# Optimization experiments

Measured on AMD Instinct MI355X. Metric: run time of the kernel, lower is better.

## Reference

```python
import jax, jax.numpy as jnp
import numpy as np

N_R = 256          # number of relations
N_HOP_MAX = 3      # max hops
N_E = 200_000      # number of entities
N_T = 1_000_000    # number of KB triples
B = 32             # batch size
D_Q = 768          # BERT question embedding dim
D_IN = D_Q + (N_HOP_MAX - 1) * N_R  # input width of dense_inf / dense_att


def setup_inputs() -> dict:
    key = jax.random.key(0)
    ks = jax.random.split(key, 7)
    x = (jax.random.uniform(ks[0], (B, N_E)) < 0.001).astype(jnp.float32)
    h_q = jax.random.normal(ks[1], (B, D_Q), jnp.float32)
    W_inf = jax.random.normal(ks[2], (N_R, D_IN), jnp.float32) * 0.02
    W_att = jax.random.normal(ks[3], (1, D_IN), jnp.float32) * 0.02
    subj_idx = jax.random.randint(ks[4], (N_T,), 0, N_E, jnp.int32)
    rel_idx = jax.random.randint(ks[5], (N_T,), 0, N_R, jnp.int32)
    obj_idx = jax.random.randint(ks[6], (N_T,), 0, N_E, jnp.int32)
    return {"x": x, "h_q": h_q, "W_inf": W_inf, "W_att": W_att,
            "subj_idx": subj_idx, "rel_idx": rel_idx, "obj_idx": obj_idx,
            "n_hop": N_HOP_MAX}


def _one_step(x, r, subj_idx, rel_idx, obj_idx):
    # Equivalent to ((x @ M_subj.T) * (r @ M_rel.T)) @ M_obj with 0/1
    # indicator matrices: gather - elementwise multiply - scatter-add.
    x_t = jnp.take(x, subj_idx, axis=1)   # (B, N_T)
    r_t = jnp.take(r, rel_idx, axis=1)    # (B, N_T)
    prod = x_t * r_t                       # (B, N_T)
    # scatter-add over triples into object entities: (N_T, B) -> (N_E, B)
    return jax.ops.segment_sum(prod.T, obj_idx, num_segments=x.shape[1]).T


def reference(x, h_q, W_inf, W_att, subj_idx, rel_idx, obj_idx, n_hop):
    rs, cs, xs = [], [], []
    for i in range(n_hop):
        if i:
            # most-recent relation first, then older ones (rs[::-1])
            concat = jnp.concatenate([h_q] + rs[::-1], axis=1)
        else:
            concat = h_q
        pad = jnp.zeros((h_q.shape[0], (N_HOP_MAX - 1 - i) * N_R), h_q.dtype)
        concat = jnp.concatenate([concat, pad], axis=1)  # (B, D_IN)
        r = concat @ W_inf.T   # (B, N_R)
        c = concat @ W_att.T   # (B, 1)
        x = _one_step(x, r, subj_idx, rel_idx, obj_idx)  # (B, N_E)
        rs.append(r)
        cs.append(c)
        xs.append(x)
    a = jax.nn.softmax(jnp.concatenate(cs, axis=1), axis=-1)  # (B, n_hop)
    y = jnp.einsum('bh,bhe->be', a, jnp.stack(xs, axis=1))     # (B, N_E)
    return y
```

## Files before the change

kernel.cpp:

```cpp
#include <hip/hip_runtime.h>

#define N_R   256
#define N_E   200000
#define N_T   1000000
#define D_Q   768
#define D_IN  1280

template <bool BN>
__device__ __forceinline__ void hop_core(
        const float* __restrict__ xIn, const unsigned* __restrict__ maskIn,
        const float* __restrict__ rT,
        const int* __restrict__ subj, const int* __restrict__ rel,
        const int* __restrict__ obj,
        float* __restrict__ xOut, unsigned* __restrict__ maskOut,
        int gb, int nGroups, int t) {
    int stride = nGroups * 256;
    for (int i = gb * 256 + t; i < N_T; i += stride) {
        int s = __builtin_nontemporal_load(&subj[i]);
        unsigned m = maskIn[s];
        if (!m) continue;
        int r = __builtin_nontemporal_load(&rel[i]);
        int o = __builtin_nontemporal_load(&obj[i]);
        const float* rrow = rT + r * 32;
        unsigned mm = m;
        while (mm) {
            int bb = __ffs(mm) - 1;
            mm &= mm - 1;
            float v = BN ? xIn[(size_t)bb * N_E + s] : xIn[(size_t)s * 32 + bb];
            unsafeAtomicAdd(&xOut[(size_t)o * 32 + bb], v * rrow[bb]);
        }
        atomicOr(&maskOut[o], m);
    }
}

__global__ void kA(const float* __restrict__ x, const float* __restrict__ h_q,
                   const float* __restrict__ W_inf,
                   unsigned* __restrict__ mask0, unsigned* __restrict__ mask1,
                   unsigned* __restrict__ mask2,
                   float4* __restrict__ outv, float* __restrict__ rT0) {
    __shared__ float hs[32 * 257];
    __shared__ float red[256];
    int t = threadIdx.x;
    if (blockIdx.x < 782) {
        int tid = blockIdx.x * 256 + t;
        float4 z = {0.f, 0.f, 0.f, 0.f};
        for (int i = tid; i < 1600000; i += 782 * 256) outv[i] = z;
        if (tid < N_E) {
            unsigned m = 0;
#pragma unroll 8
            for (int b = 0; b < 32; ++b)
                m |= (x[(size_t)b * N_E + tid] != 0.f ? 1u : 0u) << b;
            mask0[tid] = m;
            mask1[tid] = 0u;
            mask2[tid] = 0u;
        }
    } else {
        int rel = blockIdx.x - 782;
        int b = t & 31, kp = t >> 5;
        float acc = 0.f;
        for (int c = 0; c < 3; ++c) {
            __syncthreads();
#pragma unroll
            for (int i = 0; i < 32; ++i)
                hs[i * 257 + t] = h_q[i * D_Q + c * 256 + t];
            __syncthreads();
            const float* w = &W_inf[rel * D_IN + c * 256 + kp * 32];
#pragma unroll
            for (int i = 0; i < 32; ++i)
                acc += w[i] * hs[b * 257 + kp * 32 + i];
        }
        red[t] = acc;
        __syncthreads();
        if (t < 32) {
            float s = 0.f;
            for (int q = 0; q < 8; ++q) s += red[q * 32 + t];
            rT0[rel * 32 + t] = s;
        }
    }
}

__global__ void kB(const float* __restrict__ W_inf, const float* __restrict__ rT0,
                   float* __restrict__ rT1,
                   const float* __restrict__ x, const unsigned* __restrict__ mask0,
                   const int* __restrict__ subj, const int* __restrict__ rel,
                   const int* __restrict__ obj,
                   float* __restrict__ bufA, unsigned* __restrict__ mask1) {
    __shared__ float red[256];
    int t = threadIdx.x;
    if (blockIdx.x < 256) {
        int relb = blockIdx.x;
        int b = t & 31, jp = t >> 5;
        const float* w2 = &W_inf[relb * D_IN + D_Q];
        float acc = 0.f;
#pragma unroll 8
        for (int jj = 0; jj < 32; ++jj) {
            int j = jp * 32 + jj;
            acc += w2[j] * rT0[j * 32 + b];
        }
        red[t] = acc;
        __syncthreads();
        if (t < 32) {
            float s = rT0[relb * 32 + t];
            for (int q = 0; q < 8; ++q) s += red[q * 32 + t];
            rT1[relb * 32 + t] = s;
        }
    } else {
        hop_core<true>(x, mask0, rT0, subj, rel, obj, bufA, mask1,
                       blockIdx.x - 256, 2048, t);
    }
}

__global__ void kC(const float* __restrict__ W_inf, const float* __restrict__ W_att,
                   const float* __restrict__ h_q,
                   const float* __restrict__ rT0, const float* __restrict__ rT1,
                   float* __restrict__ rT2, float* __restrict__ a_w,
                   const float* __restrict__ bufA, const unsigned* __restrict__ mask1,
                   const int* __restrict__ subj, const int* __restrict__ rel,
                   const int* __restrict__ obj,
                   float* __restrict__ bufB, unsigned* __restrict__ mask2) {
    __shared__ float red[256];
    __shared__ float p0[256], p1[256], p2[256], p3[256];
    int t = threadIdx.x;
    if (blockIdx.x < 256) {
        int relb = blockIdx.x;
        int b = t & 31, jp = t >> 5;
        const float* w2 = &W_inf[relb * D_IN + D_Q];
        const float* w3 = w2 + N_R;
        float acc = 0.f;
#pragma unroll 8
        for (int jj = 0; jj < 32; ++jj) {
            int j = jp * 32 + jj;
            acc += w2[j] * rT1[j * 32 + b] + w3[j] * rT0[j * 32 + b];
        }
        red[t] = acc;
        __syncthreads();
        if (t < 32) {
            float s = rT0[relb * 32 + t];
            for (int q = 0; q < 8; ++q) s += red[q * 32 + t];
            rT2[relb * 32 + t] = s;
        }
    } else if (blockIdx.x == 256) {
        int b = t & 31, p = t >> 5;
        float c0 = 0.f;
        for (int k = p * 96; k < p * 96 + 96; ++k) c0 += W_att[k] * h_q[b * D_Q + k];
        float s1 = 0.f, s2 = 0.f, s3 = 0.f;
        for (int j = p * 32; j < p * 32 + 32; ++j) {
            float w2 = W_att[D_Q + j], w3 = W_att[D_Q + N_R + j];
            float r0v = rT0[j * 32 + b], r1v = rT1[j * 32 + b];
            s1 += w2 * r0v; s2 += w2 * r1v; s3 += w3 * r0v;
        }
        p0[t] = c0; p1[t] = s1; p2[t] = s2; p3[t] = s3;
        __syncthreads();
        if (t < 32) {
            float C0 = 0.f, S1 = 0.f, S2 = 0.f, S3 = 0.f;
            for (int q = 0; q < 8; ++q) {
                C0 += p0[q * 32 + t]; S1 += p1[q * 32 + t];
                S2 += p2[q * 32 + t]; S3 += p3[q * 32 + t];
            }
            float c1 = C0 + S1, c2 = C0 + S2 + S3;
            float m  = fmaxf(C0, fmaxf(c1, c2));
            float e0 = __expf(C0 - m), e1 = __expf(c1 - m), e2 = __expf(c2 - m);
            float inv = 1.f / (e0 + e1 + e2);
            a_w[t] = e0 * inv; a_w[32 + t] = e1 * inv; a_w[64 + t] = e2 * inv;
        }
    } else {
        hop_core<false>(bufA, mask1, rT1, subj, rel, obj, bufB, mask2,
                        blockIdx.x - 257, 2048, t);
    }
}

__global__ void kDE(const float* __restrict__ bufA, const float* __restrict__ bufB,
                    const unsigned* __restrict__ mask2, const float* __restrict__ rT2,
                    const float* __restrict__ a_w,
                    const int4* __restrict__ subj4, const int4* __restrict__ rel4,
                    const int4* __restrict__ obj4, float* __restrict__ out) {
    __shared__ float tile[32 * 65];
    __shared__ float a0s[32], a1s[32], aws[32];
    int t = threadIdx.x;
    if (blockIdx.x < 977) {
        if (t < 32) aws[t] = a_w[64 + t];
        __syncthreads();
        int tid = blockIdx.x * 256 + t;
        if (tid >= N_T / 4) return;
        int4 s4 = subj4[tid];
        unsigned m0 = mask2[s4.x], m1 = mask2[s4.y];
        unsigned m2 = mask2[s4.z], m3 = mask2[s4.w];
        if (!(m0 | m1 | m2 | m3)) return;
        int4 r4 = rel4[tid];
        int4 o4 = obj4[tid];
        int      ss[4] = {s4.x, s4.y, s4.z, s4.w};
        unsigned mk[4] = {m0, m1, m2, m3};
        int      rr[4] = {r4.x, r4.y, r4.z, r4.w};
        int      oo[4] = {o4.x, o4.y, o4.z, o4.w};
#pragma unroll
        for (int k = 0; k < 4; ++k) {
            unsigned mm = mk[k];
            if (!mm) continue;
            const float* rrow = rT2 + rr[k] * 32;
            const float* xrow = bufB + (size_t)ss[k] * 32;
            int o = oo[k];
            while (mm) {
                int bb = __ffs(mm) - 1;
                mm &= mm - 1;
                float v = xrow[bb];
                unsafeAtomicAdd(&out[(size_t)bb * N_E + o],
                                aws[bb] * v * rrow[bb]);
            }
        }
    } else {
        if (t < 32) { a0s[t] = a_w[t]; a1s[t] = a_w[32 + t]; }
        __syncthreads();
        int e0 = (blockIdx.x - 977) * 64;
#pragma unroll
        for (int i = 0; i < 8; ++i) {
            int o = i * 256 + t;
            int e = o >> 5, b = o & 31;
            size_t idx = (size_t)(e0 + e) * 32 + b;
            tile[b * 65 + e] = a0s[b] * bufA[idx] + a1s[b] * bufB[idx];
        }
        __syncthreads();
#pragma unroll
        for (int i = 0; i < 8; ++i) {
            int o = i * 256 + t;
            int b = o >> 6, e = o & 63;
            unsafeAtomicAdd(&out[(size_t)b * N_E + e0 + e], tile[b * 65 + e]);
        }
    }
}

extern "C" void kernel_launch(void* const* d_in, const int* in_sizes, int n_in,
                              void* d_out, int out_size, void* d_ws, size_t ws_size,
                              hipStream_t stream) {
    const float* x     = (const float*)d_in[0];
    const float* h_q   = (const float*)d_in[1];
    const float* W_inf = (const float*)d_in[2];
    const float* W_att = (const float*)d_in[3];
    const int*   subj  = (const int*)d_in[4];
    const int*   rel   = (const int*)d_in[5];
    const int*   obj   = (const int*)d_in[6];
    float* out = (float*)d_out;

    const size_t NEB = (size_t)N_E * 32;
    float*    bufA  = (float*)d_ws;
    float*    bufB  = bufA + NEB;
    float*    rT0   = bufB + NEB;
    float*    rT1   = rT0 + N_R * 32;
    float*    rT2   = rT1 + N_R * 32;
    float*    a_w   = rT2 + N_R * 32;
    unsigned* mask0 = (unsigned*)(a_w + 96);
    unsigned* mask1 = mask0 + N_E;
    unsigned* mask2 = mask1 + N_E;

    kA<<<782 + 256, 256, 0, stream>>>(x, h_q, W_inf, mask0, mask1, mask2,
                                      (float4*)out, rT0);
    kB<<<256 + 2048, 256, 0, stream>>>(W_inf, rT0, rT1, x, mask0,
                                       subj, rel, obj, bufA, mask1);
    kC<<<257 + 2048, 256, 0, stream>>>(W_inf, W_att, h_q, rT0, rT1, rT2, a_w,
                                       bufA, mask1, subj, rel, obj, bufB, mask2);
    kDE<<<977 + 3125, 256, 0, stream>>>(bufA, bufB, mask2, rT2, a_w,
                                        (const int4*)subj, (const int4*)rel,
                                        (const int4*)obj, out);
}
```

Baseline: 203.2 us.

## Vectorize hop triple loads to int4 and mask-skip the final blend

The hop kernels for hops 1 and 2 now give each thread four triples, read as int4 vectors. A thread checks all four subject masks and exits early when none are active, replacing the grid-stride scalar loop. The final blend of hop-1 and hop-2 results now runs one thread per entity and uses the activity masks to skip inactive entities and batch entries, instead of a dense transpose of all 6.4M entries through shared memory. This cuts bandwidth for the sparse blend, but writes become scattered uncoalesced atomics and the kernels have fewer blocks.

After: 195.6 us, median of 2. 1.04x faster.

```diff
diff --git a/kernel.cpp b/kernel.cpp
--- a/kernel.cpp
+++ b/kernel.cpp
@@ -7,29 +7,38 @@
 #define D_IN  1280
 
 template <bool BN>
-__device__ __forceinline__ void hop_core(
+__device__ __forceinline__ void hop_quad(
         const float* __restrict__ xIn, const unsigned* __restrict__ maskIn,
         const float* __restrict__ rT,
-        const int* __restrict__ subj, const int* __restrict__ rel,
-        const int* __restrict__ obj,
+        const int4* __restrict__ subj4, const int4* __restrict__ rel4,
+        const int4* __restrict__ obj4,
         float* __restrict__ xOut, unsigned* __restrict__ maskOut,
-        int gb, int nGroups, int t) {
-    int stride = nGroups * 256;
-    for (int i = gb * 256 + t; i < N_T; i += stride) {
-        int s = __builtin_nontemporal_load(&subj[i]);
-        unsigned m = maskIn[s];
-        if (!m) continue;
-        int r = __builtin_nontemporal_load(&rel[i]);
-        int o = __builtin_nontemporal_load(&obj[i]);
-        const float* rrow = rT + r * 32;
-        unsigned mm = m;
+        int gb, int t) {
+    int tid = gb * 256 + t;
+    if (tid >= N_T / 4) return;
+    int4 s4 = subj4[tid];
+    unsigned m0 = maskIn[s4.x], m1 = maskIn[s4.y];
+    unsigned m2 = maskIn[s4.z], m3 = maskIn[s4.w];
+    if (!(m0 | m1 | m2 | m3)) return;
+    int4 r4 = rel4[tid];
+    int4 o4 = obj4[tid];
+    int      ss[4] = {s4.x, s4.y, s4.z, s4.w};
+    unsigned mk[4] = {m0, m1, m2, m3};
+    int      rr[4] = {r4.x, r4.y, r4.z, r4.w};
+    int      oo[4] = {o4.x, o4.y, o4.z, o4.w};
+#pragma unroll
+    for (int k = 0; k < 4; ++k) {
+        unsigned mm = mk[k];
+        if (!mm) continue;
+        int s = ss[k], o = oo[k];
+        const float* rrow = rT + rr[k] * 32;
         while (mm) {
             int bb = __ffs(mm) - 1;
             mm &= mm - 1;
             float v = BN ? xIn[(size_t)bb * N_E + s] : xIn[(size_t)s * 32 + bb];
             unsafeAtomicAdd(&xOut[(size_t)o * 32 + bb], v * rrow[bb]);
         }
-        atomicOr(&maskOut[o], m);
+        atomicOr(&maskOut[o], mk[k]);
     }
 }
 
@@ -82,8 +91,8 @@
 __global__ void kB(const float* __restrict__ W_inf, const float* __restrict__ rT0,
                    float* __restrict__ rT1,
                    const float* __restrict__ x, const unsigned* __restrict__ mask0,
-                   const int* __restrict__ subj, const int* __restrict__ rel,
-                   const int* __restrict__ obj,
+                   const int4* __restrict__ subj4, const int4* __restrict__ rel4,
+                   const int4* __restrict__ obj4,
                    float* __restrict__ bufA, unsigned* __restrict__ mask1) {
     __shared__ float red[256];
     int t = threadIdx.x;
@@ -105,8 +114,8 @@
             rT1[relb * 32 + t] = s;
         }
     } else {
-        hop_core<true>(x, mask0, rT0, subj, rel, obj, bufA, mask1,
-                       blockIdx.x - 256, 2048, t);
+        hop_quad<true>(x, mask0, rT0, subj4, rel4, obj4, bufA, mask1,
+                       blockIdx.x - 256, t);
     }
 }
 
@@ -115,8 +124,8 @@
                    const float* __restrict__ rT0, const float* __restrict__ rT1,
                    float* __restrict__ rT2, float* __restrict__ a_w,
                    const float* __restrict__ bufA, const unsigned* __restrict__ mask1,
-                   const int* __restrict__ subj, const int* __restrict__ rel,
-                   const int* __restrict__ obj,
+                   const int4* __restrict__ subj4, const int4* __restrict__ rel4,
+                   const int4* __restrict__ obj4,
                    float* __restrict__ bufB, unsigned* __restrict__ mask2) {
     __shared__ float red[256];
     __shared__ float p0[256], p1[256], p2[256], p3[256];
@@ -164,22 +173,22 @@
             a_w[t] = e0 * inv; a_w[32 + t] = e1 * inv; a_w[64 + t] = e2 * inv;
         }
     } else {
-        hop_core<false>(bufA, mask1, rT1, subj, rel, obj, bufB, mask2,
-                        blockIdx.x - 257, 2048, t);
+        hop_quad<false>(bufA, mask1, rT1, subj4, rel4, obj4, bufB, mask2,
+                        blockIdx.x - 257, t);
     }
 }
 
 __global__ void kDE(const float* __restrict__ bufA, const float* __restrict__ bufB,
-                    const unsigned* __restrict__ mask2, const float* __restrict__ rT2,
-                    const float* __restrict__ a_w,
+                    const unsigned* __restrict__ mask1,
+                    const unsigned* __restrict__ mask2,
+                    const float* __restrict__ rT2, const float* __restrict__ a_w,
                     const int4* __restrict__ subj4, const int4* __restrict__ rel4,
                     const int4* __restrict__ obj4, float* __restrict__ out) {
-    __shared__ float tile[32 * 65];
-    __shared__ float a0s[32], a1s[32], aws[32];
-    int t = threadIdx.x;
+    __shared__ float a0s[32], a1s[32], a2s[32];
+    int t = threadIdx.x;
+    if (t < 32) { a0s[t] = a_w[t]; a1s[t] = a_w[32 + t]; a2s[t] = a_w[64 + t]; }
+    __syncthreads();
     if (blockIdx.x < 977) {
-        if (t < 32) aws[t] = a_w[64 + t];
-        __syncthreads();
         int tid = blockIdx.x * 256 + t;
         if (tid >= N_T / 4) return;
         int4 s4 = subj4[tid];
@@ -202,28 +211,25 @@
             while (mm) {
                 int bb = __ffs(mm) - 1;
                 mm &= mm - 1;
-                float v = xrow[bb];
                 unsafeAtomicAdd(&out[(size_t)bb * N_E + o],
-                                aws[bb] * v * rrow[bb]);
+                                a2s[bb] * xrow[bb] * rrow[bb]);
             }
         }
     } else {
-        if (t < 32) { a0s[t] = a_w[t]; a1s[t] = a_w[32 + t]; }
-        __syncthreads();
-        int e0 = (blockIdx.x - 977) * 64;
-#pragma unroll
-        for (int i = 0; i < 8; ++i) {
-            int o = i * 256 + t;
-            int e = o >> 5, b = o & 31;
-            size_t idx = (size_t)(e0 + e) * 32 + b;
-            tile[b * 65 + e] = a0s[b] * bufA[idx] + a1s[b] * bufB[idx];
-        }
-        __syncthreads();
-#pragma unroll
-        for (int i = 0; i < 8; ++i) {
-            int o = i * 256 + t;
-            int b = o >> 6, e = o & 63;
-            unsafeAtomicAdd(&out[(size_t)b * N_E + e0 + e], tile[b * 65 + e]);
+        int e = (blockIdx.x - 977) * 256 + t;
+        if (e >= N_E) return;
+        unsigned m1v = mask1[e], m2v = mask2[e];
+        unsigned mu = m1v | m2v;
+        if (!mu) return;
+        const float* r1 = bufA + (size_t)e * 32;
+        const float* r2 = bufB + (size_t)e * 32;
+        while (mu) {
+            int bb = __ffs(mu) - 1;
+            mu &= mu - 1;
+            float c = 0.f;
+            if ((m1v >> bb) & 1) c += a0s[bb] * r1[bb];
+            if ((m2v >> bb) & 1) c += a1s[bb] * r2[bb];
+            unsafeAtomicAdd(&out[(size_t)bb * N_E + e], c);
         }
     }
 }
@@ -253,11 +259,14 @@
 
     kA<<<782 + 256, 256, 0, stream>>>(x, h_q, W_inf, mask0, mask1, mask2,
                                       (float4*)out, rT0);
-    kB<<<256 + 2048, 256, 0, stream>>>(W_inf, rT0, rT1, x, mask0,
-                                       subj, rel, obj, bufA, mask1);
-    kC<<<257 + 2048, 256, 0, stream>>>(W_inf, W_att, h_q, rT0, rT1, rT2, a_w,
-                                       bufA, mask1, subj, rel, obj, bufB, mask2);
-    kDE<<<977 + 3125, 256, 0, stream>>>(bufA, bufB, mask2, rT2, a_w,
-                                        (const int4*)subj, (const int4*)rel,
-                                        (const int4*)obj, out);
-}
+    kB<<<256 + 977, 256, 0, stream>>>(W_inf, rT0, rT1, x, mask0,
+                                      (const int4*)subj, (const int4*)rel,
+                                      (const int4*)obj, bufA, mask1);
+    kC<<<257 + 977, 256, 0, stream>>>(W_inf, W_att, h_q, rT0, rT1, rT2, a_w,
+                                      bufA, mask1, (const int4*)subj,
+                                      (const int4*)rel, (const int4*)obj,
+                                      bufB, mask2);
+    kDE<<<977 + 782, 256, 0, stream>>>(bufA, bufB, mask1, mask2, rT2, a_w,
+                                       (const int4*)subj, (const int4*)rel,
+                                       (const int4*)obj, out);
+}
```
